# Performance work log

Measured on AMD Instinct MI355X. Metric: run time of the kernel, lower is better.

Reference implementation:

```python
import jax, jax.numpy as jnp
import numpy as np

BIG_DELTA = 1e10  # matches torch code's 1e10 sentinel for the last sample interval


def setup_inputs() -> dict:
    key = jax.random.key(0)
    k1, k2, k3 = jax.random.split(key, 3)
    num_rays, num_points = 65536, 192
    # strictly increasing depths along each ray (deltas > 0 assert in torch code)
    steps = jax.random.uniform(k1, (num_rays, num_points), jnp.float32, 0.01, 0.1)
    depth_values = jnp.cumsum(steps, axis=1)
    density = jax.random.uniform(k2, (num_rays, num_points, 1), jnp.float32)  # >= 0
    feature = jax.random.uniform(k3, (num_rays, num_points, 3), jnp.float32)
    return {"depth_values": depth_values, "density": density, "feature": feature}


def reference(depth_values, density, feature):
    # deltas: (R, P, 1); last interval is a huge sentinel as in the torch code
    deltas = jnp.concatenate(
        [depth_values[:, 1:] - depth_values[:, :-1],
         jnp.full_like(depth_values[:, :1], BIG_DELTA)], axis=1)[..., None]
    tm = deltas * density                        # (R, P, 1)
    T_i = jnp.exp(-jnp.cumsum(tm, axis=1))       # transmittance
    w_i = T_i * (1.0 - jnp.exp(-tm))             # compositing weights (R, P, 1)
    feat = jnp.sum(w_i * feature, axis=1)        # (R, 3)
    depth = jnp.sum(w_i * depth_values[..., None], axis=1)  # (R, 1)
    return jnp.concatenate([feat, depth], axis=-1)  # (R, 4) = [rgb, depth]
```

## Files before the change

### kernel.cpp

```cpp
#include <hip/hip_runtime.h>

#define BIG_DELTA 1e10f
#define P 192

__global__ __launch_bounds__(256) void volrender_kernel(
    const float* __restrict__ depth,
    const float* __restrict__ density,
    const float* __restrict__ feature,
    float* __restrict__ out,
    int num_rays)
{
    const int lane = threadIdx.x & 63;
    const int ray  = blockIdx.x * (blockDim.x >> 6) + (threadIdx.x >> 6);
    if (ray >= num_rays) return;

    const int ll = (lane < 48) ? lane : 47;

    const float4* dP = (const float4*)(depth   + (size_t)ray * P);
    const float4* sP = (const float4*)(density + (size_t)ray * P);
    const float4* fP = (const float4*)(feature + (size_t)ray * P * 3);

    float4 d  = dP[ll];
    float4 s  = sP[ll];
    float4 f0 = fP[ll * 3 + 0];
    float4 f1 = fP[ll * 3 + 1];
    float4 f2 = fP[ll * 3 + 2];

    if (lane >= 48) s = make_float4(0.f, 0.f, 0.f, 0.f);

    float dn = __shfl_down(d.x, 1);
    float delta0 = d.y - d.x;
    float delta1 = d.z - d.y;
    float delta2 = d.w - d.z;
    float delta3 = (lane == 47) ? BIG_DELTA : (dn - d.w);

    float tm0 = delta0 * s.x;
    float tm1 = delta1 * s.y;
    float tm2 = delta2 * s.z;
    float tm3 = delta3 * s.w;

    float p0 = tm0;
    float p1 = p0 + tm1;
    float p2 = p1 + tm2;
    float p3 = p2 + tm3;

    float c = p3;
    #pragma unroll
    for (int off = 1; off < 64; off <<= 1) {
        float u = __shfl_up(c, off);
        if (lane >= off) c += u;
    }
    float excl = __shfl_up(c, 1);
    if (lane == 0) excl = 0.0f;

    float w0 = __expf(-(excl + p0)) * (1.0f - __expf(-tm0));
    float w1 = __expf(-(excl + p1)) * (1.0f - __expf(-tm1));
    float w2 = __expf(-(excl + p2)) * (1.0f - __expf(-tm2));
    float w3 = __expf(-(excl + p3)) * (1.0f - __expf(-tm3));

    float accR = w0 * f0.x + w1 * f0.w + w2 * f1.z + w3 * f2.y;
    float accG = w0 * f0.y + w1 * f1.x + w2 * f1.w + w3 * f2.z;
    float accB = w0 * f0.z + w1 * f1.y + w2 * f2.x + w3 * f2.w;
    float accD = w0 * d.x  + w1 * d.y  + w2 * d.z  + w3 * d.w;

    #pragma unroll
    for (int off = 32; off > 0; off >>= 1) {
        accR += __shfl_xor(accR, off);
        accG += __shfl_xor(accG, off);
        accB += __shfl_xor(accB, off);
        accD += __shfl_xor(accD, off);
    }

    if (lane == 0) {
        ((float4*)out)[ray] = make_float4(accR, accG, accB, accD);
    }
}

extern "C" void kernel_launch(void* const* d_in, const int* in_sizes, int n_in,
                              void* d_out, int out_size, void* d_ws, size_t ws_size,
                              hipStream_t stream) {
    const float* depth   = (const float*)d_in[0];
    const float* density = (const float*)d_in[1];
    const float* feature = (const float*)d_in[2];
    float* out = (float*)d_out;

    int num_rays = in_sizes[0] / P;
    const int waves_per_block = 4;
    int blocks = (num_rays + waves_per_block - 1) / waves_per_block;
    volrender_kernel<<<blocks, 256, 0, stream>>>(depth, density, feature, out, num_rays);
}
```

Before: 41.22 us.

## Spread 3 samples per lane across all 64 lanes and split reduction across channels

Each wave now maps 3 samples per lane over all 64 lanes, replacing the layout of 4 samples per lane with 16 idle lanes, so no lanes are masked out. Loads become scalar dword loads at stride 3/9 instead of float4 vector loads. The final reduction first combines the four channels within groups of 4 lanes, then reduces a single value per lane across groups, which cuts the number of cross-lane shuffles. The cost is more load instructions that are less well vectorised.

```diff
diff --git a/kernel.cpp b/kernel.cpp
--- a/kernel.cpp
+++ b/kernel.cpp
@@ -14,37 +14,30 @@
     const int ray  = blockIdx.x * (blockDim.x >> 6) + (threadIdx.x >> 6);
     if (ray >= num_rays) return;
 
-    const int ll = (lane < 48) ? lane : 47;
+    const float* dP = depth   + (size_t)ray * P + 3 * lane;
+    const float* sP = density + (size_t)ray * P + 3 * lane;
+    const float* fP = feature + (size_t)ray * (P * 3) + 9 * lane;
 
-    const float4* dP = (const float4*)(depth   + (size_t)ray * P);
-    const float4* sP = (const float4*)(density + (size_t)ray * P);
-    const float4* fP = (const float4*)(feature + (size_t)ray * P * 3);
+    float d0 = dP[0], d1 = dP[1], d2 = dP[2];
+    float s0 = sP[0], s1 = sP[1], s2 = sP[2];
+    float f0 = fP[0], f1 = fP[1], f2 = fP[2];
+    float f3 = fP[3], f4 = fP[4], f5 = fP[5];
+    float f6 = fP[6], f7 = fP[7], f8 = fP[8];
 
-    float4 d  = dP[ll];
-    float4 s  = sP[ll];
-    float4 f0 = fP[ll * 3 + 0];
-    float4 f1 = fP[ll * 3 + 1];
-    float4 f2 = fP[ll * 3 + 2];
+    float dn = __shfl_down(d0, 1);
+    float delta0 = d1 - d0;
+    float delta1 = d2 - d1;
+    float delta2 = (lane == 63) ? BIG_DELTA : (dn - d2);
 
-    if (lane >= 48) s = make_float4(0.f, 0.f, 0.f, 0.f);
-
-    float dn = __shfl_down(d.x, 1);
-    float delta0 = d.y - d.x;
-    float delta1 = d.z - d.y;
-    float delta2 = d.w - d.z;
-    float delta3 = (lane == 47) ? BIG_DELTA : (dn - d.w);
-
-    float tm0 = delta0 * s.x;
-    float tm1 = delta1 * s.y;
-    float tm2 = delta2 * s.z;
-    float tm3 = delta3 * s.w;
+    float tm0 = delta0 * s0;
+    float tm1 = delta1 * s1;
+    float tm2 = delta2 * s2;
 
     float p0 = tm0;
     float p1 = p0 + tm1;
     float p2 = p1 + tm2;
-    float p3 = p2 + tm3;
 
-    float c = p3;
+    float c = p2;
     #pragma unroll
     for (int off = 1; off < 64; off <<= 1) {
         float u = __shfl_up(c, off);
@@ -56,24 +49,26 @@
     float w0 = __expf(-(excl + p0)) * (1.0f - __expf(-tm0));
     float w1 = __expf(-(excl + p1)) * (1.0f - __expf(-tm1));
     float w2 = __expf(-(excl + p2)) * (1.0f - __expf(-tm2));
-    float w3 = __expf(-(excl + p3)) * (1.0f - __expf(-tm3));
 
-    float accR = w0 * f0.x + w1 * f0.w + w2 * f1.z + w3 * f2.y;
-    float accG = w0 * f0.y + w1 * f1.x + w2 * f1.w + w3 * f2.z;
-    float accB = w0 * f0.z + w1 * f1.y + w2 * f2.x + w3 * f2.w;
-    float accD = w0 * d.x  + w1 * d.y  + w2 * d.z  + w3 * d.w;
+    float accR = w0 * f0 + w1 * f3 + w2 * f6;
+    float accG = w0 * f1 + w1 * f4 + w2 * f7;
+    float accB = w0 * f2 + w1 * f5 + w2 * f8;
+    float accD = w0 * d0 + w1 * d1 + w2 * d2;
 
     #pragma unroll
-    for (int off = 32; off > 0; off >>= 1) {
+    for (int off = 1; off <= 2; off <<= 1) {
         accR += __shfl_xor(accR, off);
         accG += __shfl_xor(accG, off);
         accB += __shfl_xor(accB, off);
         accD += __shfl_xor(accD, off);
     }
-
-    if (lane == 0) {
-        ((float4*)out)[ray] = make_float4(accR, accG, accB, accD);
+    const int m = lane & 3;
+    float v = (m == 0) ? accR : (m == 1) ? accG : (m == 2) ? accB : accD;
+    #pragma unroll
+    for (int off = 4; off < 64; off <<= 1) {
+        v += __shfl_xor(v, off);
     }
+    if (lane < 4) out[(size_t)ray * 4 + lane] = v;
 }
 
 extern "C" void kernel_launch(void* const* d_in, const int* in_sizes, int n_in,
```

Result: no change. 41.65 us (+1.0%).
